# Kernel optimization log

Hardware: AMD Instinct MI355X
Metric: run time of the kernel (lower is better)

## Reference

```python
import jax, jax.numpy as jnp
import numpy as np

N = 6000        # nodes
F_IN = 300      # input feature dim
HID = 128       # per-head hidden dim
H = 8           # heads
NEG_INF = -9e15 # mask value used by dense GAT
ALPHA = 0.2     # LeakyReLU slope

# NOTE: dropout (p=0.6) is applied in torch only when training=True; this
# reference implements eval mode, so all dropouts are identity.

def setup_inputs() -> dict:
    key = jax.random.key(0)
    k1, k2, k3, k4, k5, k6 = jax.random.split(key, 6)
    x = jax.random.normal(k1, (N, F_IN), dtype=jnp.float32)
    # sparse-ish 0/1 dense adjacency with self-loops (row-normalizable mask)
    adj = (jax.random.uniform(k2, (N, N)) < 0.05).astype(jnp.float32)
    adj = jnp.maximum(adj, jnp.eye(N, dtype=jnp.float32))
    # per-head params: W ~ xavier_uniform, a ~ xavier_uniform ([2*HID, 1])
    def xavier(k, shape):
        fan_in, fan_out = shape[-2], shape[-1]
        lim = jnp.sqrt(6.0 / (fan_in + fan_out)).astype(jnp.float32)
        return jax.random.uniform(k, shape, jnp.float32, -lim, lim)
    W_heads = xavier(k3, (H, F_IN, HID))          # 8 attention heads
    a_heads = xavier(k4, (H, 2 * HID, 1))
    W_out = xavier(k5, (H * HID, HID))            # final GAT layer
    a_out = xavier(k6, (2 * HID, 1))
    return {"x": x, "adj": adj, "W_heads": W_heads, "a_heads": a_heads,
            "W_out": W_out, "a_out": a_out}


def _masked_softmax(e, adj):
    # attention = softmax over rows, restricted to adj > 0
    return jax.nn.softmax(jnp.where(adj > 0, e, NEG_INF), axis=-1)


def reference(x, adj, W_heads, a_heads, W_out, a_out):
    # ---- multi-head dense GAT layer (concat=True) ----
    Wh = jnp.einsum('nf,hfo->hno', x, W_heads)                    # [H,N,O]
    a1 = a_heads[:, :HID, 0]                                      # [H,O]
    a2 = a_heads[:, HID:, 0]                                      # [H,O]
    f1 = jnp.einsum('hno,ho->hn', Wh, a1)                         # [H,N]
    f2 = jnp.einsum('hno,ho->hn', Wh, a2)                         # [H,N]
    e = jax.nn.leaky_relu(f1[:, :, None] + f2[:, None, :], ALPHA) # [H,N,N]
    attn = _masked_softmax(e, adj[None])                          # [H,N,N]
    h = jax.nn.elu(jnp.einsum('hnm,hmo->hno', attn, Wh))          # [H,N,O]
    hcat = jnp.transpose(h, (1, 0, 2)).reshape(N, H * HID)        # [N,H*O]

    # ---- final GAT layer (concat=False, no elu) ----
    Wh2 = hcat @ W_out                                            # [N,O]
    g1 = (Wh2 @ a_out[:HID]).squeeze(-1)                          # [N]
    g2 = (Wh2 @ a_out[HID:]).squeeze(-1)                          # [N]
    e2 = jax.nn.leaky_relu(g1[:, None] + g2[None, :], ALPHA)      # [N,N]
    attn2 = _masked_softmax(e2, adj)                              # [N,N]
    out = attn2 @ Wh2                                             # [N,O]
    return out
```

## Files before the change

### kernel.cpp

```cpp
#include <hip/hip_runtime.h>
#include <hip/hip_fp16.h>
#include <math.h>

#define N 6000
#define FIN 300
#define HID 128
#define NH 8
#define ALPHA 0.2f
#define NBR_CAP 512
#define KSPLIT 4
#define KPAD 384

typedef unsigned short u16;
typedef unsigned int u32;
typedef short bf16x8 __attribute__((ext_vector_type(8)));
typedef float f32x4 __attribute__((ext_vector_type(4)));

static __device__ __forceinline__ u16 f2bf(float f) {
    u32 u = __float_as_uint(f);
    u32 r = (u + 0x7fff + ((u >> 16) & 1)) >> 16;
    return (u16)r;
}
static __device__ __forceinline__ u16 f2h(float f) {
    return __half_as_ushort(__float2half(f));
}

#define PREP_NBLK (6000 + 9000 + 1536 + 512 + 8)
__global__ void prep_all(const float* __restrict__ adj,
                         const float* __restrict__ x,
                         const float* __restrict__ W,
                         const float* __restrict__ W_out,
                         const float* __restrict__ a_heads,
                         u16* __restrict__ nbr, int* __restrict__ ncnt,
                         u16* __restrict__ xb,
                         u16* __restrict__ WbT,
                         u16* __restrict__ WoT,
                         float* __restrict__ av1, float* __restrict__ av2) {
    int bid = blockIdx.x, t = threadIdx.x;
    __shared__ u16 lbuf[4][256];
    __shared__ int wc[4];
    __shared__ float a1s[HID], a2s[HID];
    if (bid < 6000) {
        int n = bid;
        int lane = t & 63, w = t >> 6;
        const int seg = N / 4;
        int start = w * seg, end = start + seg;
        const float* row = adj + (size_t)n * N;
        int cnt = 0;
        for (int base = start; base < end; base += 256) {
            int m0 = base + 4 * lane;
            float4 v = make_float4(0.f, 0.f, 0.f, 0.f);
            if (m0 < end) v = *(const float4*)(row + m0);
#pragma unroll
            for (int c = 0; c < 4; c++) {
                float vc = (c == 0) ? v.x : (c == 1) ? v.y : (c == 2) ? v.z : v.w;
                bool p = vc > 0.5f;
                unsigned long long mask = __ballot(p);
                if (p) {
                    int pos = cnt + __popcll(mask & ((1ull << lane) - 1ull));
                    if (pos < 256) lbuf[w][pos] = (u16)(m0 + c);
                }
                cnt += __popcll(mask);
            }
        }
        if (cnt > 256) cnt = 256;
        if (lane == 0) wc[w] = cnt;
        __syncthreads();
        int offset = 0;
        for (int i = 0; i < w; i++) offset += wc[i];
        for (int i = lane; i < cnt; i += 64) {
            int idx = offset + i;
            if (idx < NBR_CAP) nbr[(size_t)n * NBR_CAP + idx] = lbuf[w][i];
        }
        if (t == 0) {
            int total = wc[0] + wc[1] + wc[2] + wc[3];
            ncnt[n] = total < NBR_CAP ? total : NBR_CAP;
        }
    } else if (bid < 6000 + 9000) {
        int idx = (bid - 6000) * 256 + t;
        int n = idx / KPAD, k = idx - n * KPAD;
        xb[idx] = (k < FIN) ? f2bf(x[(size_t)n * FIN + k]) : (u16)0;
    } else if (bid < 6000 + 9000 + 1536) {
        int idx = (bid - 6000 - 9000) * 256 + t;
        int k = idx % KPAD;
        int c = (idx / KPAD) & 127;
        int h = idx / (KPAD * HID);
        WbT[idx] = (k < FIN) ? f2bf(W[((size_t)h * FIN + k) * HID + c]) : (u16)0;
    } else if (bid < 6000 + 9000 + 1536 + 512) {
        int idx = (bid - 6000 - 9000 - 1536) * 256 + t;
        int k = idx & 1023, c = idx >> 10;
        WoT[idx] = f2bf(W_out[(size_t)k * HID + c]);
    } else {
        int h = bid - (6000 + 9000 + 1536 + 512);
        if (t < HID) {
            a1s[t] = a_heads[(size_t)h * 2 * HID + t];
            a2s[t] = a_heads[(size_t)h * 2 * HID + HID + t];
        }
        __syncthreads();
        for (int f = t; f < 320; f += 256) {
            float s1 = 0.f, s2 = 0.f;
            if (f < FIN) {
                const float* wr = W + ((size_t)h * FIN + f) * HID;
#pragma unroll 4
                for (int o = 0; o < HID; o++) { s1 += wr[o] * a1s[o]; s2 += wr[o] * a2s[o]; }
            }
            av1[h * 320 + f] = s1;
            av2[h * 320 + f] = s2;
        }
    }
}

__global__ void calc_f(const float* __restrict__ x,
                       const float* __restrict__ av1, const float* __restrict__ av2,
                       float* __restrict__ f1, float* __restrict__ f2) {
    int n = blockIdx.x, t = threadIdx.x;
    int lane = t & 63, w = t >> 6;
    __shared__ float xsh[320];
    for (int i = t; i < 320; i += 256)
        xsh[i] = (i < FIN) ? x[(size_t)n * FIN + i] : 0.f;
    __syncthreads();
#pragma unroll
    for (int hh = 0; hh < 2; hh++) {
        int h = 2 * w + hh;
        const float* a1 = av1 + h * 320;
        const float* a2 = av2 + h * 320;
        float s1 = 0.f, s2 = 0.f;
#pragma unroll
        for (int i = 0; i < 5; i++) {
            float xv = xsh[lane + 64 * i];
            s1 += xv * a1[lane + 64 * i];
            s2 += xv * a2[lane + 64 * i];
        }
        for (int d = 1; d <= 32; d <<= 1) { s1 += __shfl_xor(s1, d); s2 += __shfl_xor(s2, d); }
        if (lane == 0) { f1[h * N + n] = s1; f2[h * N + n] = s2; }
    }
}

__global__ __launch_bounds__(256)
void gemm_wh_mfma(const u16* __restrict__ xb,
                  const u16* __restrict__ WbT,
                  u16* __restrict__ Whb) {
    int n0 = blockIdx.x * 64;
    int h = blockIdx.y;
    int t = threadIdx.x;
    int lane = t & 63, wid = t >> 6;
    int l4 = lane >> 4, lr = lane & 15;

    __shared__ u16 Bt[128][128];

    f32x4 acc[8];
#pragma unroll
    for (int ct = 0; ct < 8; ct++) acc[ct] = (f32x4){0.f, 0.f, 0.f, 0.f};

    int arow = n0 + 16 * wid + lr;
    const u16* asrc = xb + (size_t)arow * KPAD;
    bool avalid = (arow < N);

    for (int half = 0; half < 3; half++) {
        int kbeg = half * 128;
        {
            int c = t >> 1, sh = t & 1;
            const u16* src = WbT + ((size_t)h * HID + c) * KPAD + kbeg + sh * 64;
            int cx = (c & 7) << 3;
            uint4 v[8];
#pragma unroll
            for (int j = 0; j < 8; j++) v[j] = ((const uint4*)src)[j];
#pragma unroll
            for (int j = 0; j < 8; j++)
                *(uint4*)&Bt[c][(sh * 64 + 8 * j) ^ cx] = v[j];
        }
        __syncthreads();
#pragma unroll
        for (int kst = 0; kst < 4; kst++) {
            int kb = kst * 32 + 8 * l4;
            bf16x8 a = {0, 0, 0, 0, 0, 0, 0, 0};
            if (avalid) a = *(const bf16x8*)(asrc + kbeg + kb);
#pragma unroll
            for (int ct = 0; ct < 8; ct++) {
                int brow = 16 * ct + lr;
                bf16x8 b = *(const bf16x8*)&Bt[brow][kb ^ ((brow & 7) << 3)];
                acc[ct] = __builtin_amdgcn_mfma_f32_16x16x32_bf16(a, b, acc[ct], 0, 0, 0);
            }
        }
        __syncthreads();
    }
#pragma unroll
    for (int reg = 0; reg < 4; reg++) {
        int n = n0 + 16 * wid + 4 * l4 + reg;
        if (n < N) {
            u16* orow = Whb + ((size_t)h * N + n) * HID;
#pragma unroll
            for (int ct = 0; ct < 8; ct++)
                orow[16 * ct + lr] = f2bf(acc[ct][reg]);
        }
    }
}

__global__ void gat1(const u16* __restrict__ Whb,
                     const float* __restrict__ f1, const float* __restrict__ f2,
                     const u16* __restrict__ nbr,
                     const int* __restrict__ ncnt,
                     u16* __restrict__ hcatb) {
    int bid = blockIdx.x;
    int h = bid / N, n = bid - h * N;
    int t = threadIdx.x;
    int s = t >> 4, op = t & 15;
    int cnt = ncnt[n];
    const u16* lst = nbr + (size_t)n * NBR_CAP;
    __shared__ float2 wm[NBR_CAP];
    __shared__ float accl[16][16][9];
    __shared__ float red4[4];

    float f1c = f1[h * N + n];
    float pw = 0.f;
    for (int i = t; i < cnt; i += 256) {
        int m = lst[i];
        float z = f1c + f2[h * N + m];
        z = (z >= 0.f) ? z : ALPHA * z;
        float wv = __expf(z);
        pw += wv;
        wm[i] = make_float2(wv, __uint_as_float((u32)m << 8));
    }
    for (int d = 1; d <= 32; d <<= 1) pw += __shfl_xor(pw, d);
    if ((t & 63) == 0) red4[t >> 6] = pw;
    __syncthreads();
    float swt = red4[0] + red4[1] + red4[2] + red4[3];

    const char* base = (const char*)(Whb + (size_t)h * N * HID) + (op << 4);
    float acc[8] = {};
    int j = s;
    for (; j + 16 < cnt; j += 32) {
        float2 p0 = wm[j];
        float2 p1 = wm[j + 16];
        const uint4 va = *(const uint4*)(base + __float_as_uint(p0.y));
        const uint4 vb = *(const uint4*)(base + __float_as_uint(p1.y));
        float w0 = p0.x, w1 = p1.x;
        acc[0] += w0 * __uint_as_float(va.x << 16);
        acc[1] += w0 * __uint_as_float(va.x);
        acc[2] += w0 * __uint_as_float(va.y << 16);
        acc[3] += w0 * __uint_as_float(va.y);
        acc[4] += w0 * __uint_as_float(va.z << 16);
        acc[5] += w0 * __uint_as_float(va.z);
        acc[6] += w0 * __uint_as_float(va.w << 16);
        acc[7] += w0 * __uint_as_float(va.w);
        acc[0] += w1 * __uint_as_float(vb.x << 16);
        acc[1] += w1 * __uint_as_float(vb.x);
        acc[2] += w1 * __uint_as_float(vb.y << 16);
        acc[3] += w1 * __uint_as_float(vb.y);
        acc[4] += w1 * __uint_as_float(vb.z << 16);
        acc[5] += w1 * __uint_as_float(vb.z);
        acc[6] += w1 * __uint_as_float(vb.w << 16);
        acc[7] += w1 * __uint_as_float(vb.w);
    }
    if (j < cnt) {
        float2 p0 = wm[j];
        const uint4 va = *(const uint4*)(base + __float_as_uint(p0.y));
        float w0 = p0.x;
        acc[0] += w0 * __uint_as_float(va.x << 16);
        acc[1] += w0 * __uint_as_float(va.x);
        acc[2] += w0 * __uint_as_float(va.y << 16);
        acc[3] += w0 * __uint_as_float(va.y);
        acc[4] += w0 * __uint_as_float(va.z << 16);
        acc[5] += w0 * __uint_as_float(va.z);
        acc[6] += w0 * __uint_as_float(va.w << 16);
        acc[7] += w0 * __uint_as_float(va.w);
    }
#pragma unroll
    for (int c = 0; c < 8; c++) accl[s][op][c] = acc[c];
    __syncthreads();

    if (t < 128) {
        int c = t;
        float r = 0.f;
#pragma unroll
        for (int k = 0; k < 16; k++) r += accl[k][c >> 3][c & 7];
        r /= swt;
        r = (r > 0.f) ? r : expm1f(r);
        hcatb[(size_t)n * (NH * HID) + h * HID + c] = f2bf(r);
    }
}

__global__ __launch_bounds__(256)
void gemm_out_mfma(const u16* __restrict__ hcatb,
                   const u16* __restrict__ WoT,
                   float* __restrict__ partial) {
    int n0 = blockIdx.x * 64;
    int ks = blockIdx.y;
    int t = threadIdx.x;
    int lane = t & 63, wid = t >> 6;
    int l4 = lane >> 4, lr = lane & 15;

    __shared__ u16 Bt[128][128];

    f32x4 acc[8];
#pragma unroll
    for (int ct = 0; ct < 8; ct++) acc[ct] = (f32x4){0.f, 0.f, 0.f, 0.f};

    int arow = n0 + 16 * wid + lr;
    const u16* asrc = hcatb + (size_t)arow * (NH * HID);
    bool avalid = (arow < N);

    for (int half = 0; half < 2; half++) {
        int kbeg = ks * 256 + half * 128;
        {
            int c = t >> 1, sh = t & 1;
            const u16* src = WoT + (size_t)c * 1024 + kbeg + sh * 64;
            int cx = (c & 7) << 3;
            uint4 v[8];
#pragma unroll
            for (int j = 0; j < 8; j++) v[j] = ((const uint4*)src)[j];
#pragma unroll
            for (int j = 0; j < 8; j++)
                *(uint4*)&Bt[c][(sh * 64 + 8 * j) ^ cx] = v[j];
        }
        __syncthreads();
#pragma unroll
        for (int kst = 0; kst < 4; kst++) {
            int kb = kst * 32 + 8 * l4;
            bf16x8 a = {0, 0, 0, 0, 0, 0, 0, 0};
            if (avalid) a = *(const bf16x8*)(asrc + kbeg + kb);
#pragma unroll
            for (int ct = 0; ct < 8; ct++) {
                int brow = 16 * ct + lr;
                bf16x8 b = *(const bf16x8*)&Bt[brow][kb ^ ((brow & 7) << 3)];
                acc[ct] = __builtin_amdgcn_mfma_f32_16x16x32_bf16(a, b, acc[ct], 0, 0, 0);
            }
        }
        __syncthreads();
    }
    float* pout = partial + (size_t)ks * N * HID;
#pragma unroll
    for (int reg = 0; reg < 4; reg++) {
        int n = n0 + 16 * wid + 4 * l4 + reg;
        if (n < N) {
#pragma unroll
            for (int ct = 0; ct < 8; ct++)
                pout[(size_t)n * HID + 16 * ct + lr] = acc[ct][reg];
        }
    }
}

__global__ void reduce_wh2(const float* __restrict__ partial,
                           const float* __restrict__ a_out,
                           u16* __restrict__ Wh2h,
                           float* __restrict__ g1, float* __restrict__ g2) {
    int idx = blockIdx.x * 256 + threadIdx.x;
    float4 v = *(const float4*)(partial + 4 * (size_t)idx);
#pragma unroll
    for (int s = 1; s < KSPLIT; s++) {
        const float4 q = *(const float4*)(partial + (size_t)s * N * HID + 4 * (size_t)idx);
        v.x += q.x; v.y += q.y; v.z += q.z; v.w += q.w;
    }
    ushort4 h4;
    h4.x = f2h(v.x); h4.y = f2h(v.y); h4.z = f2h(v.z); h4.w = f2h(v.w);
    *(ushort4*)(Wh2h + 4 * (size_t)idx) = h4;

    int row = idx >> 5, cg = idx & 31;
    float p1 = v.x * a_out[4 * cg] + v.y * a_out[4 * cg + 1]
             + v.z * a_out[4 * cg + 2] + v.w * a_out[4 * cg + 3];
    float p2 = v.x * a_out[HID + 4 * cg] + v.y * a_out[HID + 4 * cg + 1]
             + v.z * a_out[HID + 4 * cg + 2] + v.w * a_out[HID + 4 * cg + 3];
    for (int d = 1; d <= 16; d <<= 1) { p1 += __shfl_xor(p1, d); p2 += __shfl_xor(p2, d); }
    if ((threadIdx.x & 31) == 0) { g1[row] = p1; g2[row] = p2; }
}

__global__ void gat2(const u16* __restrict__ Wh2h,
                     const float* __restrict__ g1, const float* __restrict__ g2,
                     const u16* __restrict__ nbr,
                     const int* __restrict__ ncnt,
                     float* __restrict__ out) {
    int n = blockIdx.x, t = threadIdx.x;
    int s = t >> 4, op = t & 15;
    int cnt = ncnt[n];
    const u16* lst = nbr + (size_t)n * NBR_CAP;
    __shared__ float2 wm[NBR_CAP];
    __shared__ float accl[16][16][9];
    __shared__ float red4[4];

    float g1c = g1[n];
    float pw = 0.f;
    for (int i = t; i < cnt; i += 256) {
        int m = lst[i];
        float z = g1c + g2[m];
        z = (z >= 0.f) ? z : ALPHA * z;
        float wv = __expf(z);
        pw += wv;
        wm[i] = make_float2(wv, __uint_as_float((u32)m << 8));
    }
    for (int d = 1; d <= 32; d <<= 1) pw += __shfl_xor(pw, d);
    if ((t & 63) == 0) red4[t >> 6] = pw;
    __syncthreads();
    float swt = red4[0] + red4[1] + red4[2] + red4[3];

    const char* base = (const char*)Wh2h + (op << 4);
    float acc[8] = {};
    int j = s;
    for (; j + 16 < cnt; j += 32) {
        float2 p0 = wm[j];
        float2 p1 = wm[j + 16];
        const uint4 va = *(const uint4*)(base + __float_as_uint(p0.y));
        const uint4 vb = *(const uint4*)(base + __float_as_uint(p1.y));
        float w0 = p0.x, w1 = p1.x;
        acc[0] += w0 * __half2float(__ushort_as_half((u16)(va.x & 0xffff)));
        acc[1] += w0 * __half2float(__ushort_as_half((u16)(va.x >> 16)));
        acc[2] += w0 * __half2float(__ushort_as_half((u16)(va.y & 0xffff)));
        acc[3] += w0 * __half2float(__ushort_as_half((u16)(va.y >> 16)));
        acc[4] += w0 * __half2float(__ushort_as_half((u16)(va.z & 0xffff)));
        acc[5] += w0 * __half2float(__ushort_as_half((u16)(va.z >> 16)));
        acc[6] += w0 * __half2float(__ushort_as_half((u16)(va.w & 0xffff)));
        acc[7] += w0 * __half2float(__ushort_as_half((u16)(va.w >> 16)));
        acc[0] += w1 * __half2float(__ushort_as_half((u16)(vb.x & 0xffff)));
        acc[1] += w1 * __half2float(__ushort_as_half((u16)(vb.x >> 16)));
        acc[2] += w1 * __half2float(__ushort_as_half((u16)(vb.y & 0xffff)));
        acc[3] += w1 * __half2float(__ushort_as_half((u16)(vb.y >> 16)));
        acc[4] += w1 * __half2float(__ushort_as_half((u16)(vb.z & 0xffff)));
        acc[5] += w1 * __half2float(__ushort_as_half((u16)(vb.z >> 16)));
        acc[6] += w1 * __half2float(__ushort_as_half((u16)(vb.w & 0xffff)));
        acc[7] += w1 * __half2float(__ushort_as_half((u16)(vb.w >> 16)));
    }
    if (j < cnt) {
        float2 p0 = wm[j];
        const uint4 va = *(const uint4*)(base + __float_as_uint(p0.y));
        float w0 = p0.x;
        acc[0] += w0 * __half2float(__ushort_as_half((u16)(va.x & 0xffff)));
        acc[1] += w0 * __half2float(__ushort_as_half((u16)(va.x >> 16)));
        acc[2] += w0 * __half2float(__ushort_as_half((u16)(va.y & 0xffff)));
        acc[3] += w0 * __half2float(__ushort_as_half((u16)(va.y >> 16)));
        acc[4] += w0 * __half2float(__ushort_as_half((u16)(va.z & 0xffff)));
        acc[5] += w0 * __half2float(__ushort_as_half((u16)(va.z >> 16)));
        acc[6] += w0 * __half2float(__ushort_as_half((u16)(va.w & 0xffff)));
        acc[7] += w0 * __half2float(__ushort_as_half((u16)(va.w >> 16)));
    }
#pragma unroll
    for (int c = 0; c < 8; c++) accl[s][op][c] = acc[c];
    __syncthreads();

    if (t < 128) {
        int c = t;
        float r = 0.f;
#pragma unroll
        for (int k = 0; k < 16; k++) r += accl[k][c >> 3][c & 7];
        out[(size_t)n * HID + c] = r / swt;
    }
}

extern "C" void kernel_launch(void* const* d_in, const int* in_sizes, int n_in,
                              void* d_out, int out_size, void* d_ws, size_t ws_size,
                              hipStream_t stream) {
    const float* x       = (const float*)d_in[0];
    const float* adj     = (const float*)d_in[1];
    const float* W_heads = (const float*)d_in[2];
    const float* a_heads = (const float*)d_in[3];
    const float* W_out   = (const float*)d_in[4];
    const float* a_out   = (const float*)d_in[5];
    float* out = (float*)d_out;

    char* wsb = (char*)d_ws;
    size_t off = 0;
    auto alloc = [&](size_t bytes) {
        void* p = wsb + off;
        off += (bytes + 255) & ~(size_t)255;
        return p;
    };
    float* partial = (float*)alloc(sizeof(float) * (size_t)KSPLIT * N * HID);
    u16*   Whb  = (u16*)  alloc(sizeof(u16)   * (size_t)NH * N * HID);
    u16*   hcatb= (u16*)  alloc(sizeof(u16)   * (size_t)N * NH * HID);
    u16*   xb   = (u16*)  alloc(sizeof(u16)   * (size_t)N * KPAD);
    u16*   WbT  = (u16*)  alloc(sizeof(u16)   * (size_t)NH * HID * KPAD);
    u16*   WoT  = (u16*)  alloc(sizeof(u16)   * (size_t)HID * 1024);
    u16*   Wh2h = (u16*)  alloc(sizeof(u16)   * (size_t)N * HID);
    float* av1  = (float*)alloc(sizeof(float) * (size_t)NH * 320);
    float* av2  = (float*)alloc(sizeof(float) * (size_t)NH * 320);
    float* f1   = (float*)alloc(sizeof(float) * (size_t)NH * N);
    float* f2   = (float*)alloc(sizeof(float) * (size_t)NH * N);
    float* g1   = (float*)alloc(sizeof(float) * (size_t)N);
    float* g2   = (float*)alloc(sizeof(float) * (size_t)N);
    u16* nbr    = (u16*)  alloc(sizeof(u16)   * (size_t)N * NBR_CAP);
    int* ncnt   = (int*)  alloc(sizeof(int)   * (size_t)N);

    hipLaunchKernelGGL(prep_all, dim3(PREP_NBLK), dim3(256), 0, stream,
                       adj, x, W_heads, W_out, a_heads, nbr, ncnt, xb, WbT, WoT, av1, av2);
    hipLaunchKernelGGL(calc_f, dim3(N), dim3(256), 0, stream, x, av1, av2, f1, f2);
    hipLaunchKernelGGL(gemm_wh_mfma, dim3((N + 63) / 64, NH), dim3(256), 0, stream,
                       xb, WbT, Whb);
    hipLaunchKernelGGL(gat1, dim3(NH * N), dim3(256), 0, stream, Whb, f1, f2, nbr, ncnt, hcatb);
    hipLaunchKernelGGL(gemm_out_mfma, dim3((N + 63) / 64, KSPLIT), dim3(256), 0, stream,
                       hcatb, WoT, partial);
    hipLaunchKernelGGL(reduce_wh2, dim3(N * HID / 4 / 256), dim3(256), 0, stream,
                       partial, a_out, Wh2h, g1, g2);
    hipLaunchKernelGGL(gat2, dim3(N), dim3(256), 0, stream, Wh2h, g1, g2, nbr, ncnt, out);
}
```

Measured before the change: 278.8 us.

## Replace sparse gather GAT1 aggregation with dense bitmask-masked MFMA attention

Replaces the per-node neighbor-gather aggregation in the first GAT layer with a dense tiled kernel. It computes masked exp weights from an adjacency bitmask into shared memory as bf16 and multiplies them against a transposed Wh with MFMA instructions, iterating over all 6000 columns. A new bitmask-building kernel and a transposed Wh GEMM output layout support this. The cost is doing dense work over roughly 20x more entries than the 5% sparsity requires, in exchange for matrix-core throughput and coalesced loads. Attention weights are also rounded to bf16, which lowers precision.

```diff
diff --git a/kernel.cpp b/kernel.cpp
--- a/kernel.cpp
+++ b/kernel.cpp
@@ -10,6 +10,8 @@
 #define NBR_CAP 512
 #define KSPLIT 4
 #define KPAD 384
+#define NWORDS 188
+#define NCH 94
 
 typedef unsigned short u16;
 typedef unsigned int u32;
@@ -110,6 +112,23 @@
     }
 }
 
+__global__ void build_bitmask(const u16* __restrict__ nbr,
+                              const int* __restrict__ ncnt,
+                              u32* __restrict__ adjb) {
+    int n = blockIdx.x, t = threadIdx.x;
+    __shared__ u32 bm[NWORDS];
+    if (t < NWORDS) bm[t] = 0;
+    __syncthreads();
+    int cnt = ncnt[n];
+    const u16* lst = nbr + (size_t)n * NBR_CAP;
+    for (int i = t; i < cnt; i += 256) {
+        int m = lst[i];
+        atomicOr(&bm[m >> 5], 1u << (m & 31));
+    }
+    __syncthreads();
+    if (t < NWORDS) adjb[(size_t)n * NWORDS + t] = bm[t];
+}
+
 __global__ void calc_f(const float* __restrict__ x,
                        const float* __restrict__ av1, const float* __restrict__ av2,
                        float* __restrict__ f1, float* __restrict__ f2) {
@@ -137,9 +156,9 @@
 }
 
 __global__ __launch_bounds__(256)
-void gemm_wh_mfma(const u16* __restrict__ xb,
-                  const u16* __restrict__ WbT,
-                  u16* __restrict__ Whb) {
+void gemm_whT_mfma(const u16* __restrict__ xb,
+                   const u16* __restrict__ WbT,
+                   u16* __restrict__ WhbT) {
     int n0 = blockIdx.x * 64;
     int h = blockIdx.y;
     int t = threadIdx.x;
@@ -148,13 +167,12 @@
 
     __shared__ u16 Bt[128][128];
 
-    f32x4 acc[8];
-#pragma unroll
-    for (int ct = 0; ct < 8; ct++) acc[ct] = (f32x4){0.f, 0.f, 0.f, 0.f};
-
-    int arow = n0 + 16 * wid + lr;
-    const u16* asrc = xb + (size_t)arow * KPAD;
-    bool avalid = (arow < N);
+    f32x4 acc[2][4];
+#pragma unroll
+    for (int rt = 0; rt < 2; rt++)
+#pragma unroll
+        for (int ctl = 0; ctl < 4; ctl++)
+            acc[rt][ctl] = (f32x4){0.f, 0.f, 0.f, 0.f};
 
     for (int half = 0; half < 3; half++) {
         int kbeg = half * 128;
@@ -173,8 +191,112 @@
 #pragma unroll
         for (int kst = 0; kst < 4; kst++) {
             int kb = kst * 32 + 8 * l4;
-            bf16x8 a = {0, 0, 0, 0, 0, 0, 0, 0};
-            if (avalid) a = *(const bf16x8*)(asrc + kbeg + kb);
+            int axr = (lr & 7) << 3;
+            bf16x8 a0 = *(const bf16x8*)&Bt[32 * wid + lr][kb ^ axr];
+            bf16x8 a1 = *(const bf16x8*)&Bt[32 * wid + 16 + lr][kb ^ axr];
+#pragma unroll
+            for (int ctl = 0; ctl < 4; ctl++) {
+                int m = n0 + 16 * ctl + lr;
+                bf16x8 b = *(const bf16x8*)(xb + (size_t)m * KPAD + kbeg + kb);
+                acc[0][ctl] = __builtin_amdgcn_mfma_f32_16x16x32_bf16(a0, b, acc[0][ctl], 0, 0, 0);
+                acc[1][ctl] = __builtin_amdgcn_mfma_f32_16x16x32_bf16(a1, b, acc[1][ctl], 0, 0, 0);
+            }
+        }
+        __syncthreads();
+    }
+#pragma unroll
+    for (int rt = 0; rt < 2; rt++) {
+#pragma unroll
+        for (int reg = 0; reg < 4; reg++) {
+            int c = 32 * wid + 16 * rt + 4 * l4 + reg;
+            u16* orow = WhbT + ((size_t)h * HID + c) * N;
+#pragma unroll
+            for (int ctl = 0; ctl < 4; ctl++) {
+                int m = n0 + 16 * ctl + lr;
+                if (m < N) orow[m] = f2bf(acc[rt][ctl][reg]);
+            }
+        }
+    }
+}
+
+__global__ __launch_bounds__(256)
+void gat1_dense(const u16* __restrict__ WhbT,
+                const float* __restrict__ f1, const float* __restrict__ f2,
+                const u32* __restrict__ adjb,
+                u16* __restrict__ hcatb) {
+    int tile = blockIdx.x, h = blockIdx.y;
+    int n0 = tile * 64;
+    int t = threadIdx.x;
+    int lane = t & 63, wid = t >> 6;
+    int l4 = lane >> 4, lr = lane & 15;
+    int r = t >> 2, q = t & 3;
+
+    __shared__ float f2s[6016];
+    __shared__ u16 P[64][64];
+    __shared__ u16 Bt[128][64];
+    __shared__ float swl[64];
+
+    const float* f2h_ = f2 + (size_t)h * N;
+    for (int i = t; i < 6016; i += 256)
+        f2s[i] = (i < N) ? f2h_[i] : 0.f;
+    int nrow = n0 + r;
+    float f1c = (nrow < N) ? f1[h * N + nrow] : 0.f;
+    const u32* rbits = adjb + (size_t)nrow * NWORDS;
+    int xr = (r & 7) << 3;
+    const u16* bsrc = WhbT + (size_t)h * HID * N;
+    int c = t >> 1, sh = t & 1;
+    int cx = (c & 7) << 3;
+    __syncthreads();
+
+    f32x4 acc[8];
+#pragma unroll
+    for (int ct = 0; ct < 8; ct++) acc[ct] = (f32x4){0.f, 0.f, 0.f, 0.f};
+    float swp = 0.f;
+
+    for (int ch = 0; ch < NCH; ch++) {
+        int m0 = ch * 64;
+        int mb = m0 + sh * 32;
+        const u16* src = bsrc + (size_t)c * N + mb;
+        uint4 v0, v1, v2, v3;
+        if (mb + 32 <= N) {
+            v0 = ((const uint4*)src)[0]; v1 = ((const uint4*)src)[1];
+            v2 = ((const uint4*)src)[2]; v3 = ((const uint4*)src)[3];
+        } else {
+            u16 tmp[32];
+#pragma unroll
+            for (int j = 0; j < 32; j++) tmp[j] = (mb + j < N) ? src[j] : (u16)0;
+            v0 = ((const uint4*)tmp)[0]; v1 = ((const uint4*)tmp)[1];
+            v2 = ((const uint4*)tmp)[2]; v3 = ((const uint4*)tmp)[3];
+        }
+        u32 bits = rbits[ch * 2 + (q >> 1)] >> ((q & 1) * 16);
+        const float* fsrc = f2s + m0 + 16 * q;
+        u32 pw[8];
+#pragma unroll
+        for (int jp = 0; jp < 8; jp++) {
+            float s0 = f1c + fsrc[2 * jp];
+            float s1 = f1c + fsrc[2 * jp + 1];
+            float z0 = fmaxf(s0, 0.2f * s0);
+            float z1 = fmaxf(s1, 0.2f * s1);
+            float w0 = __expf(z0) * (float)((bits >> (2 * jp)) & 1);
+            float w1 = __expf(z1) * (float)((bits >> (2 * jp + 1)) & 1);
+            u32 b0 = f2bf(w0), b1 = f2bf(w1);
+            swp += __uint_as_float(b0 << 16) + __uint_as_float(b1 << 16);
+            pw[jp] = b0 | (b1 << 16);
+        }
+#pragma unroll
+        for (int jp = 0; jp < 8; jp++)
+            *(u32*)&P[r][(16 * q + 2 * jp) ^ xr] = pw[jp];
+        *(uint4*)&Bt[c][(sh * 32 + 0)  ^ cx] = v0;
+        *(uint4*)&Bt[c][(sh * 32 + 8)  ^ cx] = v1;
+        *(uint4*)&Bt[c][(sh * 32 + 16) ^ cx] = v2;
+        *(uint4*)&Bt[c][(sh * 32 + 24) ^ cx] = v3;
+        __syncthreads();
+        int arow = 16 * wid + lr;
+        int axr = (lr & 7) << 3;
+#pragma unroll
+        for (int ks = 0; ks < 2; ks++) {
+            int kb = ks * 32 + 8 * l4;
+            bf16x8 a = *(const bf16x8*)&P[arow][kb ^ axr];
 #pragma unroll
             for (int ct = 0; ct < 8; ct++) {
                 int brow = 16 * ct + lr;
@@ -184,99 +306,24 @@
         }
         __syncthreads();
     }
+    swp += __shfl_xor(swp, 1);
+    swp += __shfl_xor(swp, 2);
+    if (q == 0) swl[r] = swp;
+    __syncthreads();
 #pragma unroll
     for (int reg = 0; reg < 4; reg++) {
-        int n = n0 + 16 * wid + 4 * l4 + reg;
+        int rl = 16 * wid + 4 * l4 + reg;
+        int n = n0 + rl;
         if (n < N) {
-            u16* orow = Whb + ((size_t)h * N + n) * HID;
-#pragma unroll
-            for (int ct = 0; ct < 8; ct++)
-                orow[16 * ct + lr] = f2bf(acc[ct][reg]);
-        }
-    }
-}
-
-__global__ void gat1(const u16* __restrict__ Whb,
-                     const float* __restrict__ f1, const float* __restrict__ f2,
-                     const u16* __restrict__ nbr,
-                     const int* __restrict__ ncnt,
-                     u16* __restrict__ hcatb) {
-    int bid = blockIdx.x;
-    int h = bid / N, n = bid - h * N;
-    int t = threadIdx.x;
-    int s = t >> 4, op = t & 15;
-    int cnt = ncnt[n];
-    const u16* lst = nbr + (size_t)n * NBR_CAP;
-    __shared__ float2 wm[NBR_CAP];
-    __shared__ float accl[16][16][9];
-    __shared__ float red4[4];
-
-    float f1c = f1[h * N + n];
-    float pw = 0.f;
-    for (int i = t; i < cnt; i += 256) {
-        int m = lst[i];
-        float z = f1c + f2[h * N + m];
-        z = (z >= 0.f) ? z : ALPHA * z;
-        float wv = __expf(z);
-        pw += wv;
-        wm[i] = make_float2(wv, __uint_as_float((u32)m << 8));
-    }
-    for (int d = 1; d <= 32; d <<= 1) pw += __shfl_xor(pw, d);
-    if ((t & 63) == 0) red4[t >> 6] = pw;
-    __syncthreads();
-    float swt = red4[0] + red4[1] + red4[2] + red4[3];
-
-    const char* base = (const char*)(Whb + (size_t)h * N * HID) + (op << 4);
-    float acc[8] = {};
-    int j = s;
-    for (; j + 16 < cnt; j += 32) {
-        float2 p0 = wm[j];
-        float2 p1 = wm[j + 16];
-        const uint4 va = *(const uint4*)(base + __float_as_uint(p0.y));
-        const uint4 vb = *(const uint4*)(base + __float_as_uint(p1.y));
-        float w0 = p0.x, w1 = p1.x;
-        acc[0] += w0 * __uint_as_float(va.x << 16);
-        acc[1] += w0 * __uint_as_float(va.x);
-        acc[2] += w0 * __uint_as_float(va.y << 16);
-        acc[3] += w0 * __uint_as_float(va.y);
-        acc[4] += w0 * __uint_as_float(va.z << 16);
-        acc[5] += w0 * __uint_as_float(va.z);
-        acc[6] += w0 * __uint_as_float(va.w << 16);
-        acc[7] += w0 * __uint_as_float(va.w);
-        acc[0] += w1 * __uint_as_float(vb.x << 16);
-        acc[1] += w1 * __uint_as_float(vb.x);
-        acc[2] += w1 * __uint_as_float(vb.y << 16);
-        acc[3] += w1 * __uint_as_float(vb.y);
-        acc[4] += w1 * __uint_as_float(vb.z << 16);
-        acc[5] += w1 * __uint_as_float(vb.z);
-        acc[6] += w1 * __uint_as_float(vb.w << 16);
-        acc[7] += w1 * __uint_as_float(vb.w);
-    }
-    if (j < cnt) {
-        float2 p0 = wm[j];
-        const uint4 va = *(const uint4*)(base + __float_as_uint(p0.y));
-        float w0 = p0.x;
-        acc[0] += w0 * __uint_as_float(va.x << 16);
-        acc[1] += w0 * __uint_as_float(va.x);
-        acc[2] += w0 * __uint_as_float(va.y << 16);
-        acc[3] += w0 * __uint_as_float(va.y);
-        acc[4] += w0 * __uint_as_float(va.z << 16);
-        acc[5] += w0 * __uint_as_float(va.z);
-        acc[6] += w0 * __uint_as_float(va.w << 16);
-        acc[7] += w0 * __uint_as_float(va.w);
-    }
-#pragma unroll
-    for (int c = 0; c < 8; c++) accl[s][op][c] = acc[c];
-    __syncthreads();
-
-    if (t < 128) {
-        int c = t;
-        float r = 0.f;
-#pragma unroll
-        for (int k = 0; k < 16; k++) r += accl[k][c >> 3][c & 7];
-        r /= swt;
-        r = (r > 0.f) ? r : expm1f(r);
-        hcatb[(size_t)n * (NH * HID) + h * HID + c] = f2bf(r);
+            float inv = 1.f / swl[rl];
+            u16* orow = hcatb + (size_t)n * (NH * HID) + h * HID;
+#pragma unroll
+            for (int ct = 0; ct < 8; ct++) {
+                float v = acc[ct][reg] * inv;
+                v = (v > 0.f) ? v : expm1f(v);
+                orow[16 * ct + lr] = f2bf(v);
+            }
+        }
     }
 }
 
@@ -432,15 +479,15 @@
         acc[7] += w0 * __half2float(__ushort_as_half((u16)(va.w >> 16)));
     }
 #pragma unroll
-    for (int c = 0; c < 8; c++) accl[s][op][c] = acc[c];
+    for (int cc = 0; cc < 8; cc++) accl[s][op][cc] = acc[cc];
     __syncthreads();
 
     if (t < 128) {
-        int c = t;
+        int cc = t;
         float r = 0.f;
 #pragma unroll
-        for (int k = 0; k < 16; k++) r += accl[k][c >> 3][c & 7];
-        out[(size_t)n * HID + c] = r / swt;
+        for (int k = 0; k < 16; k++) r += accl[k][cc >> 3][cc & 7];
+        out[(size_t)n * HID + cc] = r / swt;
     }
 }
 
@@ -463,12 +510,13 @@
         return p;
     };
     float* partial = (float*)alloc(sizeof(float) * (size_t)KSPLIT * N * HID);
-    u16*   Whb  = (u16*)  alloc(sizeof(u16)   * (size_t)NH * N * HID);
+    u16*   WhbT = (u16*)  alloc(sizeof(u16)   * (size_t)NH * HID * N);
     u16*   hcatb= (u16*)  alloc(sizeof(u16)   * (size_t)N * NH * HID);
     u16*   xb   = (u16*)  alloc(sizeof(u16)   * (size_t)N * KPAD);
     u16*   WbT  = (u16*)  alloc(sizeof(u16)   * (size_t)NH * HID * KPAD);
     u16*   WoT  = (u16*)  alloc(sizeof(u16)   * (size_t)HID * 1024);
     u16*   Wh2h = (u16*)  alloc(sizeof(u16)   * (size_t)N * HID);
+    u32*   adjb = (u32*)  alloc(sizeof(u32)   * (size_t)N * NWORDS);
     float* av1  = (float*)alloc(sizeof(float) * (size_t)NH * 320);
     float* av2  = (float*)alloc(sizeof(float) * (size_t)NH * 320);
     float* f1   = (float*)alloc(sizeof(float) * (size_t)NH * N);
@@ -480,10 +528,12 @@
 
     hipLaunchKernelGGL(prep_all, dim3(PREP_NBLK), dim3(256), 0, stream,
                        adj, x, W_heads, W_out, a_heads, nbr, ncnt, xb, WbT, WoT, av1, av2);
+    hipLaunchKernelGGL(build_bitmask, dim3(N), dim3(256), 0, stream, nbr, ncnt, adjb);
     hipLaunchKernelGGL(calc_f, dim3(N), dim3(256), 0, stream, x, av1, av2, f1, f2);
-    hipLaunchKernelGGL(gemm_wh_mfma, dim3((N + 63) / 64, NH), dim3(256), 0, stream,
-                       xb, WbT, Whb);
-    hipLaunchKernelGGL(gat1, dim3(NH * N), dim3(256), 0, stream, Whb, f1, f2, nbr, ncnt, hcatb);
+    hipLaunchKernelGGL(gemm_whT_mfma, dim3((N + 63) / 64, NH), dim3(256), 0, stream,
+                       xb, WbT, WhbT);
+    hipLaunchKernelGGL(gat1_dense, dim3(NCH, NH), dim3(256), 0, stream,
+                       WhbT, f1, f2, adjb, hcatb);
     hipLaunchKernelGGL(gemm_out_mfma, dim3((N + 63) / 64, KSPLIT), dim3(256), 0, stream,
                        hcatb, WoT, partial);
     hipLaunchKernelGGL(reduce_wh2, dim3(N * HID / 4 / 256), dim3(256), 0, stream,
```

Result: slower. 335.4 us (+20.3%).
